# Optimization experiments

Hardware: AMD Instinct MI355X
Metric: run time of the kernel (lower is better)

Reference implementation:

```python
import jax, jax.numpy as jnp
import numpy as np

B, L, D, H = 4, 2048, 1024, 16
HD = D // H
NEG = -1e9  # stands in for -inf in masks; identical softmax result, grad-safe
EPS = 1e-5


def _layer_norm(x, g, b):
    mu = jnp.mean(x, axis=-1, keepdims=True)
    var = jnp.mean((x - mu) ** 2, axis=-1, keepdims=True)
    return (x - mu) * jax.lax.rsqrt(var + EPS) * g + b


def setup_inputs() -> dict:
    key = jax.random.key(0)
    ks = jax.random.split(key, 8)
    x = jax.random.normal(ks[0], (B, L, D), dtype=jnp.float32)
    # length-based padding: valid lengths in [L//2, L]; True = padded position
    lengths = jax.random.randint(ks[1], (B,), L // 2, L + 1)
    padding_mask = jnp.arange(L)[None, :] >= lengths[:, None]  # (B, L) bool
    # additive causal mask: 0 on/below diagonal, NEG above
    causal_mask = jnp.where(jnp.tril(jnp.ones((L, L), dtype=bool)), 0.0, NEG).astype(jnp.float32)

    def linear_params(k, fan_in, fan_out):
        bound = float(np.sqrt(6.0 / (fan_in + fan_out)))  # xavier_uniform
        W = jax.random.uniform(k, (fan_out, fan_in), jnp.float32, -bound, bound)
        b = jnp.zeros((fan_out,), jnp.float32)
        return W, b

    Wq, bq = linear_params(ks[2], D, D)
    Wk, bk = linear_params(ks[3], D, D)
    Wv, bv = linear_params(ks[4], D, D)
    Wo, bo = linear_params(ks[5], D, D)
    g_pre = jnp.ones((D,), jnp.float32); b_pre = jnp.zeros((D,), jnp.float32)
    g_ln = jnp.ones((D,), jnp.float32); b_ln = jnp.zeros((D,), jnp.float32)
    return {
        "x": x, "padding_mask": padding_mask, "causal_mask": causal_mask,
        "Wq": Wq, "bq": bq, "Wk": Wk, "bk": bk, "Wv": Wv, "bv": bv,
        "Wo": Wo, "bo": bo, "g_pre": g_pre, "b_pre": b_pre,
        "g_ln": g_ln, "b_ln": b_ln,
    }


def reference(x, padding_mask, causal_mask, Wq, bq, Wk, bk, Wv, bv, Wo, bo,
              g_pre, b_pre, g_ln, b_ln):
    # pre-LayerNorm (residual uses the normed x, matching the torch code)
    h = _layer_norm(x, g_pre, b_pre)  # (B, L, D)

    def heads(W, b):
        y = jnp.einsum('bld,ed->ble', h, W) + b           # torch Linear: x @ W.T + b
        return y.reshape(B, L, H, HD).transpose(0, 2, 1, 3)  # (B, H, L, HD)

    q, k, v = heads(Wq, bq), heads(Wk, bk), heads(Wv, bv)

    scores = jnp.einsum('bhld,bhmd->bhlm', q, k) / jnp.sqrt(jnp.float32(HD))
    scores = scores + causal_mask  # additive causal mask broadcast over (B, H)
    # padding mask: True = masked key position
    scores = jnp.where(padding_mask[:, None, None, :], NEG, scores)
    attn = jax.nn.softmax(scores, axis=-1)  # dropout p=0.0 (eval / disabled)

    out = jnp.einsum('bhlm,bhmd->bhld', attn, v)          # (B, H, L, HD)
    out = out.transpose(0, 2, 1, 3).reshape(B, L, D)
    out = jnp.einsum('bld,ed->ble', out, Wo) + bo
    return _layer_norm(out + h, g_ln, b_ln)
```

## Files before the change

kernel.cpp:

```cpp
#include <hip/hip_runtime.h>


#define Bq 4
#define Lq 2048
#define Dq 1024
#define Hq 16
#define HDq 64
#define Mq (Bq * Lq)

typedef __attribute__((ext_vector_type(8))) short short8;
typedef __attribute__((ext_vector_type(4))) float f32x4;
typedef __attribute__((address_space(3))) unsigned char lds_byte;
typedef __attribute__((address_space(1))) unsigned char gbl_byte;

__device__ __forceinline__ unsigned short f2b(float f) {
    unsigned int u = __float_as_uint(f);
    unsigned int r = (u + 0x7fffu + ((u >> 16) & 1u)) >> 16;
    return (unsigned short)r;
}
__device__ __forceinline__ float b2f(unsigned short u) {
    return __uint_as_float(((unsigned int)u) << 16);
}
__device__ __forceinline__ unsigned int packbf(float lo, float hi) {
    return (unsigned int)f2b(lo) | ((unsigned int)f2b(hi) << 16);
}

#define GLL16(gsrc, ldst)                                              \
    __builtin_amdgcn_global_load_lds((const gbl_byte*)(gsrc),          \
                                     (lds_byte*)(ldst), 16, 0, 0)

#define MFMA_BF16(A, B, C) \
    __builtin_amdgcn_mfma_f32_16x16x32_bf16((A), (B), (C), 0, 0, 0)

__global__ void setup_kernel(const unsigned char* __restrict__ m8,
                             int* __restrict__ lengths) {
    __shared__ int bad;
    __shared__ int fo[4];
    const int tid = threadIdx.x;
    if (tid == 0) bad = 0;
    if (tid < 4) fo[tid] = Lq;
    __syncthreads();
    for (int i = tid; i < Bq * Lq; i += 256) {
        unsigned char v = m8[i];
        if (v) {
            int r = i >> 11, c = i & (Lq - 1);
            atomicMin(&fo[r], c);
            if (c < Lq / 2) atomicOr(&bad, 1);
            else if (c < Lq - 1 && m8[i + 1] == 0) atomicOr(&bad, 1);
        }
    }
    __syncthreads();
    int anyone = (fo[0] < Lq) | (fo[1] < Lq) | (fo[2] < Lq) | (fo[3] < Lq);
    bool use8 = (bad == 0) && anyone;
    if (!use8) {
        __syncthreads();
        if (tid < 4) fo[tid] = Lq;
        __syncthreads();
        const int* m32 = (const int*)m8;
        for (int i = tid; i < Bq * Lq; i += 256) {
            if (m32[i] != 0) atomicMin(&fo[i >> 11], i & (Lq - 1));
        }
        __syncthreads();
    }
    if (tid < 4) lengths[tid] = fo[tid];
}

__global__ __launch_bounds__(256) void cvt4_kernel(
    const float* __restrict__ s0, const float* __restrict__ s1,
    const float* __restrict__ s2, const float* __restrict__ s3,
    unsigned short* __restrict__ dst) {
    const int region = blockIdx.x >> 10;
    const int i = (blockIdx.x & 1023) * 256 + threadIdx.x;
    const float* src = (region == 0) ? s0 : (region == 1) ? s1
                       : (region == 2) ? s2 : s3;
    float4 v = ((const float4*)src)[i];
    ushort4 o;
    o.x = f2b(v.x); o.y = f2b(v.y); o.z = f2b(v.z); o.w = f2b(v.w);
    ((ushort4*)dst)[(size_t)region * (Dq * Dq / 4) + i] = o;
}

__global__ __launch_bounds__(256) void ln_pre_kernel(
    const float* __restrict__ x, const float* __restrict__ g,
    const float* __restrict__ bb, unsigned short* __restrict__ out) {
    const int row = blockIdx.x, tid = threadIdx.x;
    float4 u = ((const float4*)x)[(size_t)row * 256 + tid];
    float s = u.x + u.y + u.z + u.w;
    float ss = u.x * u.x + u.y * u.y + u.z * u.z + u.w * u.w;
#pragma unroll
    for (int off = 32; off > 0; off >>= 1) {
        s += __shfl_xor(s, off);
        ss += __shfl_xor(ss, off);
    }
    __shared__ float sred[4], ssred[4];
    const int w = tid >> 6, lane = tid & 63;
    if (lane == 0) { sred[w] = s; ssred[w] = ss; }
    __syncthreads();
    s = sred[0] + sred[1] + sred[2] + sred[3];
    ss = ssred[0] + ssred[1] + ssred[2] + ssred[3];
    const float mean = s * (1.f / Dq);
    const float rstd = rsqrtf(ss * (1.f / Dq) - mean * mean + 1e-5f);
    float4 gv = ((const float4*)g)[tid];
    float4 bv = ((const float4*)bb)[tid];
    ushort4 o;
    o.x = f2b((u.x - mean) * rstd * gv.x + bv.x);
    o.y = f2b((u.y - mean) * rstd * gv.y + bv.y);
    o.z = f2b((u.z - mean) * rstd * gv.z + bv.z);
    o.w = f2b((u.w - mean) * rstd * gv.w + bv.w);
    ((ushort4*)out)[(size_t)row * 256 + tid] = o;
}

__global__ __launch_bounds__(256) void qkv_gemm_kernel(
    const unsigned short* __restrict__ A, const unsigned short* __restrict__ W3,
    const float* __restrict__ bq, const float* __restrict__ bk,
    const float* __restrict__ bv, unsigned short* __restrict__ Qo,
    unsigned short* __restrict__ Ko, unsigned short* __restrict__ Vto) {
    __shared__ unsigned short As[128][32];
    __shared__ unsigned short Bs[128][32];
    const int tid = threadIdx.x;
    const int w = tid >> 6, lane = tid & 63;
    const int lm = lane & 15, lq = lane >> 4;
    const int lin = blockIdx.y * 24 + blockIdx.x;
    const int swz = (lin & 7) * (1536 / 8) + (lin >> 3);
    const int m0 = (swz / 24) << 7, n0 = (swz % 24) << 7;
    const int wm = (w >> 1) << 6, wn = (w & 1) << 6;
    f32x4 acc[4][4];
#pragma unroll
    for (int i = 0; i < 4; ++i)
#pragma unroll
        for (int j = 0; j < 4; ++j) acc[i][j] = (f32x4){0.f, 0.f, 0.f, 0.f};
    for (int k0 = 0; k0 < Dq; k0 += 32) {
        __syncthreads();
#pragma unroll
        for (int j = 0; j < 2; ++j) {
            const int base = j * 256 + w * 64;
            const int slot = base + lane;
            const int row = slot >> 2, c = slot & 3;
            GLL16(A + (size_t)(m0 + row) * Dq + k0 + c * 8,
                  (unsigned short*)As + base * 8);
            GLL16(W3 + (size_t)(n0 + row) * Dq + k0 + c * 8,
                  (unsigned short*)Bs + base * 8);
        }
        __syncthreads();
        short8 af[4], bf[4];
#pragma unroll
        for (int t = 0; t < 4; ++t)
            af[t] = *(const short8*)&As[wm + t * 16 + lm][lq * 8];
#pragma unroll
        for (int t = 0; t < 4; ++t)
            bf[t] = *(const short8*)&Bs[wn + t * 16 + lm][lq * 8];
#pragma unroll
        for (int mt = 0; mt < 4; ++mt)
#pragma unroll
            for (int nt = 0; nt < 4; ++nt)
                acc[mt][nt] = __builtin_amdgcn_mfma_f32_16x16x32_bf16(
                    af[mt], bf[nt], acc[mt][nt], 0, 0, 0);
    }
    const int region = n0 >> 10;
    const float* bias = (region == 0) ? bq : (region == 1) ? bk : bv;
    const float scale = (region == 0) ? 0.125f : 1.0f;
    const int nb = n0 & 1023;
#pragma unroll
    for (int nt = 0; nt < 4; ++nt) {
        const int colb = nb + wn + nt * 16 + lm;
        const float bval = bias[colb];
#pragma unroll
        for (int mt = 0; mt < 4; ++mt) {
            const int row0 = m0 + wm + mt * 16 + lq * 4;
            const int bidx = row0 >> 11, l0r = row0 & (Lq - 1);
            if (region < 2) {
                unsigned short* dst = (region == 0) ? Qo : Ko;
#pragma unroll
                for (int r = 0; r < 4; ++r)
                    dst[((size_t)(bidx * Hq + (colb >> 6)) * Lq + l0r + r) *
                            HDq + (colb & 63)] =
                        f2b((acc[mt][nt][r] + bval) * scale);
            } else {
                ushort4 o;
                o.x = f2b(acc[mt][nt][0] + bval);
                o.y = f2b(acc[mt][nt][1] + bval);
                o.z = f2b(acc[mt][nt][2] + bval);
                o.w = f2b(acc[mt][nt][3] + bval);
                *(ushort4*)&Vto[((size_t)(bidx * Hq + (colb >> 6)) * HDq +
                                 (colb & 63)) * Lq + l0r] = o;
            }
        }
    }
}

__global__ __launch_bounds__(256) void proj_gemm_kernel(
    const unsigned short* __restrict__ A, const unsigned short* __restrict__ Bw,
    const float* __restrict__ bias, float* __restrict__ Cout) {
    __shared__ unsigned short As[128][32];
    __shared__ unsigned short Bs[128][32];
    const int tid = threadIdx.x;
    const int w = tid >> 6, lane = tid & 63;
    const int lm = lane & 15, lq = lane >> 4;
    const int lin = blockIdx.y * 8 + blockIdx.x;
    const int swz = (lin & 7) * (512 / 8) + (lin >> 3);
    const int m0 = (swz >> 3) << 7, n0 = (swz & 7) << 7;
    const int wm = (w >> 1) << 6, wn = (w & 1) << 6;
    f32x4 acc[4][4];
#pragma unroll
    for (int i = 0; i < 4; ++i)
#pragma unroll
        for (int j = 0; j < 4; ++j) acc[i][j] = (f32x4){0.f, 0.f, 0.f, 0.f};
    for (int k0 = 0; k0 < Dq; k0 += 32) {
        __syncthreads();
#pragma unroll
        for (int j = 0; j < 2; ++j) {
            const int base = j * 256 + w * 64;
            const int slot = base + lane;
            const int row = slot >> 2, c = slot & 3;
            const int rr = m0 + row, kk = k0 + c * 8;
            GLL16(A + ((size_t)((rr >> 11) * Hq + (kk >> 6)) * Lq +
                       (rr & (Lq - 1))) * HDq + (kk & 63),
                  (unsigned short*)As + base * 8);
            GLL16(Bw + (size_t)(n0 + row) * Dq + k0 + c * 8,
                  (unsigned short*)Bs + base * 8);
        }
        __syncthreads();
        short8 af[4], bf[4];
#pragma unroll
        for (int t = 0; t < 4; ++t)
            af[t] = *(const short8*)&As[wm + t * 16 + lm][lq * 8];
#pragma unroll
        for (int t = 0; t < 4; ++t)
            bf[t] = *(const short8*)&Bs[wn + t * 16 + lm][lq * 8];
#pragma unroll
        for (int mt = 0; mt < 4; ++mt)
#pragma unroll
            for (int nt = 0; nt < 4; ++nt)
                acc[mt][nt] = __builtin_amdgcn_mfma_f32_16x16x32_bf16(
                    af[mt], bf[nt], acc[mt][nt], 0, 0, 0);
    }
#pragma unroll
    for (int nt = 0; nt < 4; ++nt) {
        const float bval = bias[n0 + wn + nt * 16 + lm];
#pragma unroll
        for (int mt = 0; mt < 4; ++mt)
#pragma unroll
            for (int r = 0; r < 4; ++r)
                Cout[(size_t)(m0 + wm + mt * 16 + lq * 4 + r) * Dq + n0 + wn +
                     nt * 16 + lm] = acc[mt][nt][r] + bval;
    }
}

__global__ __launch_bounds__(256, 2) void attn_kernel(
    const unsigned short* __restrict__ Qg, const unsigned short* __restrict__ Kg,
    const unsigned short* __restrict__ Vtg, const int* __restrict__ lengths,
    unsigned short* __restrict__ Og) {
    __shared__ unsigned short Kbuf[2][4096];
    __shared__ unsigned short Vbuf[2][4096];
    __shared__ unsigned short Ps[4][2][16][72];
    const int bx = blockIdx.x;
    const int hh = blockIdx.y, b = blockIdx.z;
    const int tid = threadIdx.x, w = tid >> 6, lane = tid & 63;
    const int lm = lane & 15, lq = lane >> 4;
    const int len = lengths[b];
    const int mxk = (len + 63) >> 6;
    const size_t hb = (size_t)(b * Hq + hh) * Lq * HDq;
    const unsigned short* Vb = Vtg + hb;

    const int srow = w * 8 + (lane >> 3);
    const int ssw = (lane & 7) ^ (lane >> 3);
    const unsigned short* pK = Kg + hb + (size_t)srow * HDq + ssw * 8;
    const unsigned short* pV = Vb + (size_t)srow * Lq + ssw * 8;

#define STAGE_KV(BUF, KB)                                                   \
    {                                                                       \
        GLL16(pK + (size_t)(KB)*HDq, &Kbuf[(BUF)][(w * 64) * 8]);           \
        GLL16(pK + (size_t)((KB) + 32) * HDq,                               \
              &Kbuf[(BUF)][(256 + w * 64) * 8]);                            \
        GLL16(pV + (KB), &Vbuf[(BUF)][(w * 64) * 8]);                       \
        GLL16(pV + (size_t)32 * Lq + (KB),                                  \
              &Vbuf[(BUF)][(256 + w * 64) * 8]);                            \
    }

#pragma unroll
    for (int pass = 0; pass < 2; ++pass) {
        const int qt = pass ? bx : (15 - bx);
        const int l0 = qt << 7;
        short8 qf[2][2];
#pragma unroll
        for (int s = 0; s < 2; ++s)
#pragma unroll
            for (int h = 0; h < 2; ++h)
                qf[s][h] = *(const short8*)(Qg + hb +
                    (size_t)(l0 + w * 32 + s * 16 + lm) * HDq + h * 32 + lq * 8);
        f32x4 oacc[2][4];
        float m_i[2], l_i[2];
#pragma unroll
        for (int s = 0; s < 2; ++s) {
            m_i[s] = -1e30f; l_i[s] = 0.f;
#pragma unroll
            for (int t = 0; t < 4; ++t)
                oacc[s][t] = (f32x4){0.f, 0.f, 0.f, 0.f};
        }
        int nkt = 2 * qt + 2;
        if (nkt > mxk) nkt = mxk;
        STAGE_KV(0, 0);
        __syncthreads();
        for (int kt = 0; kt < nkt; ++kt) {
            const int kb = kt << 6;
            const int cur = kt & 1;
            if (kt + 1 < nkt) STAGE_KV(cur ^ 1, (kt + 1) << 6);
            short8 kf[4][2], vf[4][2];
#pragma unroll
            for (int t = 0; t < 4; ++t) {
                const int ro = (t * 16 + lm) * 64;
                const int sx = lm & 7;
#pragma unroll
                for (int h = 0; h < 2; ++h) {
                    const int off = ro + (((h * 4 + lq) ^ sx) << 3);
                    kf[t][h] = *(const short8*)&Kbuf[cur][off];
                    vf[t][h] = *(const short8*)&Vbuf[cur][off];
                }
            }
            f32x4 sc[2][4];
            __builtin_amdgcn_s_setprio(1);
#pragma unroll
            for (int s = 0; s < 2; ++s) {
#pragma unroll
                for (int t = 0; t < 4; ++t) {
                    f32x4 z = (f32x4){0.f, 0.f, 0.f, 0.f};
                    z = MFMA_BF16(kf[t][0], qf[s][0], z);
                    z = MFMA_BF16(kf[t][1], qf[s][1], z);
                    sc[s][t] = z;
                }
            }
            __builtin_amdgcn_s_setprio(0);
#pragma unroll
            for (int s = 0; s < 2; ++s) {
                const int qmin = l0 + w * 32 + s * 16;
                float pvv[16];
                float mx = -1e30f;
                if ((kb + 63 <= qmin) && (kb + 63 < len)) {
#pragma unroll
                    for (int i = 0; i < 16; ++i) {
                        const float v = sc[s][i >> 2][i & 3];
                        pvv[i] = v;
                        mx = fmaxf(mx, v);
                    }
                } else {
                    const int qq = qmin + lm;
#pragma unroll
                    for (int t = 0; t < 4; ++t)
#pragma unroll
                        for (int r = 0; r < 4; ++r) {
                            const int key = kb + t * 16 + lq * 4 + r;
                            float v = sc[s][t][r];
                            if (key > qq || key >= len) v = -1e30f;
                            pvv[t * 4 + r] = v;
                            mx = fmaxf(mx, v);
                        }
                }
                mx = fmaxf(mx, __shfl_xor(mx, 16));
                mx = fmaxf(mx, __shfl_xor(mx, 32));
                const float mnew = fmaxf(m_i[s], mx);
                float psum = 0.f;
#pragma unroll
                for (int i = 0; i < 16; ++i) {
                    const float p = __expf(pvv[i] - mnew);
                    pvv[i] = p;
                    psum += p;
                }
#pragma unroll
                for (int t = 0; t < 4; ++t) {
                    uint2 uu;
                    uu.x = packbf(pvv[t * 4 + 0], pvv[t * 4 + 1]);
                    uu.y = packbf(pvv[t * 4 + 2], pvv[t * 4 + 3]);
                    *(uint2*)&Ps[w][s][lm][t * 16 + lq * 4] = uu;
                }
                psum += __shfl_xor(psum, 16);
                psum += __shfl_xor(psum, 32);
                const float alpha = __expf(m_i[s] - mnew);
                m_i[s] = mnew;
                l_i[s] = l_i[s] * alpha + psum;
#pragma unroll
                for (int t = 0; t < 4; ++t) {
                    oacc[s][t][0] *= alpha; oacc[s][t][1] *= alpha;
                    oacc[s][t][2] *= alpha; oacc[s][t][3] *= alpha;
                }
            }
            asm volatile("s_waitcnt lgkmcnt(0)" ::: "memory");
            __builtin_amdgcn_s_setprio(1);
#pragma unroll
            for (int s = 0; s < 2; ++s) {
                short8 pf0 = *(const short8*)&Ps[w][s][lm][lq * 8];
                short8 pf1 = *(const short8*)&Ps[w][s][lm][32 + lq * 8];
#pragma unroll
                for (int t = 0; t < 4; ++t) {
                    oacc[s][t] = MFMA_BF16(vf[t][0], pf0, oacc[s][t]);
                    oacc[s][t] = MFMA_BF16(vf[t][1], pf1, oacc[s][t]);
                }
            }
            __builtin_amdgcn_s_setprio(0);
            __syncthreads();
        }
#pragma unroll
        for (int s = 0; s < 2; ++s) {
            const float inv = 1.f / l_i[s];
            unsigned short* Ot =
                Og + hb + (size_t)(l0 + w * 32 + s * 16 + lm) * HDq;
#pragma unroll
            for (int t = 0; t < 4; ++t) {
                ushort4 o;
                o.x = f2b(oacc[s][t][0] * inv);
                o.y = f2b(oacc[s][t][1] * inv);
                o.z = f2b(oacc[s][t][2] * inv);
                o.w = f2b(oacc[s][t][3] * inv);
                *(ushort4*)(Ot + t * 16 + lq * 4) = o;
            }
        }
    }
#undef STAGE_KV
}

__global__ __launch_bounds__(256) void ln_final_kernel(
    const float* __restrict__ pj, const unsigned short* __restrict__ h,
    const float* __restrict__ g, const float* __restrict__ bb,
    float* __restrict__ out) {
    const int row = blockIdx.x, tid = threadIdx.x;
    float4 a = ((const float4*)pj)[(size_t)row * 256 + tid];
    ushort4 hv = ((const ushort4*)h)[(size_t)row * 256 + tid];
    float f0 = a.x + b2f(hv.x), f1 = a.y + b2f(hv.y);
    float f2 = a.z + b2f(hv.z), f3 = a.w + b2f(hv.w);
    float s = f0 + f1 + f2 + f3;
    float ss = f0 * f0 + f1 * f1 + f2 * f2 + f3 * f3;
#pragma unroll
    for (int off = 32; off > 0; off >>= 1) {
        s += __shfl_xor(s, off);
        ss += __shfl_xor(ss, off);
    }
    __shared__ float sred[4], ssred[4];
    const int w = tid >> 6, lane = tid & 63;
    if (lane == 0) { sred[w] = s; ssred[w] = ss; }
    __syncthreads();
    s = sred[0] + sred[1] + sred[2] + sred[3];
    ss = ssred[0] + ssred[1] + ssred[2] + ssred[3];
    const float mean = s * (1.f / Dq);
    const float rstd = rsqrtf(ss * (1.f / Dq) - mean * mean + 1e-5f);
    float4 gv = ((const float4*)g)[tid];
    float4 bv = ((const float4*)bb)[tid];
    float4 o;
    o.x = (f0 - mean) * rstd * gv.x + bv.x;
    o.y = (f1 - mean) * rstd * gv.y + bv.y;
    o.z = (f2 - mean) * rstd * gv.z + bv.z;
    o.w = (f3 - mean) * rstd * gv.w + bv.w;
    ((float4*)out)[(size_t)row * 256 + tid] = o;
}

extern "C" void kernel_launch(void* const* d_in, const int* in_sizes, int n_in,
                              void* d_out, int out_size, void* d_ws,
                              size_t ws_size, hipStream_t stream) {
    const float* x = (const float*)d_in[0];
    const unsigned char* mask = (const unsigned char*)d_in[1];
    const float* Wq = (const float*)d_in[3];
    const float* bq = (const float*)d_in[4];
    const float* Wk = (const float*)d_in[5];
    const float* bk = (const float*)d_in[6];
    const float* Wv = (const float*)d_in[7];
    const float* bvv = (const float*)d_in[8];
    const float* Wo = (const float*)d_in[9];
    const float* bo = (const float*)d_in[10];
    const float* g_pre = (const float*)d_in[11];
    const float* b_pre = (const float*)d_in[12];
    const float* g_ln = (const float*)d_in[13];
    const float* b_ln = (const float*)d_in[14];

    const size_t SZ = (size_t)Mq * Dq;
    const size_t WSZ = (size_t)Dq * Dq;
    unsigned short* h = (unsigned short*)d_ws;
    unsigned short* q = h + SZ;
    unsigned short* k = q + SZ;
    unsigned short* vT = k + SZ;
    unsigned short* at = vT + SZ;
    unsigned short* W3 = at + SZ;
    unsigned short* wob = W3 + 3 * WSZ;
    float* proj = (float*)(wob + WSZ);
    int* lengths = (int*)(proj + SZ);

    setup_kernel<<<1, 256, 0, stream>>>(mask, lengths);
    cvt4_kernel<<<4096, 256, 0, stream>>>(Wq, Wk, Wv, Wo, W3);
    ln_pre_kernel<<<Mq, 256, 0, stream>>>(x, g_pre, b_pre, h);

    qkv_gemm_kernel<<<dim3(3 * Dq / 128, Mq / 128), 256, 0, stream>>>(
        h, W3, bq, bk, bvv, q, k, vT);
    attn_kernel<<<dim3(Lq / 256, Hq, Bq), 256, 0, stream>>>(q, k, vT, lengths,
                                                            at);
    proj_gemm_kernel<<<dim3(Dq / 128, Mq / 128), 256, 0, stream>>>(at, wob, bo,
                                                                   proj);
    ln_final_kernel<<<Mq, 256, 0, stream>>>(proj, h, g_ln, b_ln,
                                            (float*)d_out);
}
```

Baseline: 360.7 us.

## Double-buffer GEMM LDS tiles and remap attention blocks for XCD locality

Both the QKV and output-projection GEMMs now use two LDS buffers: the next K-slice is loaded asynchronously while MFMAs run on the current one, leaving one barrier per iteration instead of two. The attention kernel remaps its linear block index so that blocks sharing a (batch, head) land on the same XCD, which is meant to improve L2 reuse of K/V. Double buffering doubles the GEMM LDS footprint, which could reduce occupancy. The one-barrier scheme depends on the asynchronous global-to-LDS loads completing before the barrier.

```diff
diff --git a/kernel.cpp b/kernel.cpp
--- a/kernel.cpp
+++ b/kernel.cpp
@@ -114,8 +114,8 @@
     const float* __restrict__ bq, const float* __restrict__ bk,
     const float* __restrict__ bv, unsigned short* __restrict__ Qo,
     unsigned short* __restrict__ Ko, unsigned short* __restrict__ Vto) {
-    __shared__ unsigned short As[128][32];
-    __shared__ unsigned short Bs[128][32];
+    __shared__ unsigned short As[2][128][32];
+    __shared__ unsigned short Bs[2][128][32];
     const int tid = threadIdx.x;
     const int w = tid >> 6, lane = tid & 63;
     const int lm = lane & 15, lq = lane >> 4;
@@ -128,33 +128,42 @@
     for (int i = 0; i < 4; ++i)
 #pragma unroll
         for (int j = 0; j < 4; ++j) acc[i][j] = (f32x4){0.f, 0.f, 0.f, 0.f};
+
+#define QKV_STAGE(BUF, K0)                                              \
+    {                                                                   \
+        _Pragma("unroll")                                               \
+        for (int j = 0; j < 2; ++j) {                                   \
+            const int base = j * 256 + w * 64;                          \
+            const int slot = base + lane;                               \
+            const int row = slot >> 2, c = slot & 3;                    \
+            GLL16(A + (size_t)(m0 + row) * Dq + (K0) + c * 8,           \
+                  (unsigned short*)As[BUF] + base * 8);                 \
+            GLL16(W3 + (size_t)(n0 + row) * Dq + (K0) + c * 8,          \
+                  (unsigned short*)Bs[BUF] + base * 8);                 \
+        }                                                               \
+    }
+
+    QKV_STAGE(0, 0);
+    __syncthreads();
     for (int k0 = 0; k0 < Dq; k0 += 32) {
-        __syncthreads();
-#pragma unroll
-        for (int j = 0; j < 2; ++j) {
-            const int base = j * 256 + w * 64;
-            const int slot = base + lane;
-            const int row = slot >> 2, c = slot & 3;
-            GLL16(A + (size_t)(m0 + row) * Dq + k0 + c * 8,
-                  (unsigned short*)As + base * 8);
-            GLL16(W3 + (size_t)(n0 + row) * Dq + k0 + c * 8,
-                  (unsigned short*)Bs + base * 8);
-        }
-        __syncthreads();
+        const int cur = (k0 >> 5) & 1;
+        if (k0 + 32 < Dq) QKV_STAGE(cur ^ 1, k0 + 32);
         short8 af[4], bf[4];
 #pragma unroll
         for (int t = 0; t < 4; ++t)
-            af[t] = *(const short8*)&As[wm + t * 16 + lm][lq * 8];
+            af[t] = *(const short8*)&As[cur][wm + t * 16 + lm][lq * 8];
 #pragma unroll
         for (int t = 0; t < 4; ++t)
-            bf[t] = *(const short8*)&Bs[wn + t * 16 + lm][lq * 8];
+            bf[t] = *(const short8*)&Bs[cur][wn + t * 16 + lm][lq * 8];
 #pragma unroll
         for (int mt = 0; mt < 4; ++mt)
 #pragma unroll
             for (int nt = 0; nt < 4; ++nt)
                 acc[mt][nt] = __builtin_amdgcn_mfma_f32_16x16x32_bf16(
                     af[mt], bf[nt], acc[mt][nt], 0, 0, 0);
-    }
+        __syncthreads();
+    }
+#undef QKV_STAGE
     const int region = n0 >> 10;
     const float* bias = (region == 0) ? bq : (region == 1) ? bk : bv;
     const float scale = (region == 0) ? 0.125f : 1.0f;
@@ -190,8 +199,8 @@
 __global__ __launch_bounds__(256) void proj_gemm_kernel(
     const unsigned short* __restrict__ A, const unsigned short* __restrict__ Bw,
     const float* __restrict__ bias, float* __restrict__ Cout) {
-    __shared__ unsigned short As[128][32];
-    __shared__ unsigned short Bs[128][32];
+    __shared__ unsigned short As[2][128][32];
+    __shared__ unsigned short Bs[2][128][32];
     const int tid = threadIdx.x;
     const int w = tid >> 6, lane = tid & 63;
     const int lm = lane & 15, lq = lane >> 4;
@@ -204,35 +213,44 @@
     for (int i = 0; i < 4; ++i)
 #pragma unroll
         for (int j = 0; j < 4; ++j) acc[i][j] = (f32x4){0.f, 0.f, 0.f, 0.f};
+
+#define PROJ_STAGE(BUF, K0)                                             \
+    {                                                                   \
+        _Pragma("unroll")                                               \
+        for (int j = 0; j < 2; ++j) {                                   \
+            const int base = j * 256 + w * 64;                          \
+            const int slot = base + lane;                               \
+            const int row = slot >> 2, c = slot & 3;                    \
+            const int rr = m0 + row, kk = (K0) + c * 8;                 \
+            GLL16(A + ((size_t)((rr >> 11) * Hq + (kk >> 6)) * Lq +     \
+                       (rr & (Lq - 1))) * HDq + (kk & 63),              \
+                  (unsigned short*)As[BUF] + base * 8);                 \
+            GLL16(Bw + (size_t)(n0 + row) * Dq + (K0) + c * 8,          \
+                  (unsigned short*)Bs[BUF] + base * 8);                 \
+        }                                                               \
+    }
+
+    PROJ_STAGE(0, 0);
+    __syncthreads();
     for (int k0 = 0; k0 < Dq; k0 += 32) {
-        __syncthreads();
-#pragma unroll
-        for (int j = 0; j < 2; ++j) {
-            const int base = j * 256 + w * 64;
-            const int slot = base + lane;
-            const int row = slot >> 2, c = slot & 3;
-            const int rr = m0 + row, kk = k0 + c * 8;
-            GLL16(A + ((size_t)((rr >> 11) * Hq + (kk >> 6)) * Lq +
-                       (rr & (Lq - 1))) * HDq + (kk & 63),
-                  (unsigned short*)As + base * 8);
-            GLL16(Bw + (size_t)(n0 + row) * Dq + k0 + c * 8,
-                  (unsigned short*)Bs + base * 8);
-        }
-        __syncthreads();
+        const int cur = (k0 >> 5) & 1;
+        if (k0 + 32 < Dq) PROJ_STAGE(cur ^ 1, k0 + 32);
         short8 af[4], bf[4];
 #pragma unroll
         for (int t = 0; t < 4; ++t)
-            af[t] = *(const short8*)&As[wm + t * 16 + lm][lq * 8];
+            af[t] = *(const short8*)&As[cur][wm + t * 16 + lm][lq * 8];
 #pragma unroll
         for (int t = 0; t < 4; ++t)
-            bf[t] = *(const short8*)&Bs[wn + t * 16 + lm][lq * 8];
+            bf[t] = *(const short8*)&Bs[cur][wn + t * 16 + lm][lq * 8];
 #pragma unroll
         for (int mt = 0; mt < 4; ++mt)
 #pragma unroll
             for (int nt = 0; nt < 4; ++nt)
                 acc[mt][nt] = __builtin_amdgcn_mfma_f32_16x16x32_bf16(
                     af[mt], bf[nt], acc[mt][nt], 0, 0, 0);
-    }
+        __syncthreads();
+    }
+#undef PROJ_STAGE
 #pragma unroll
     for (int nt = 0; nt < 4; ++nt) {
         const float bval = bias[n0 + wn + nt * 16 + lm];
@@ -252,8 +270,11 @@
     __shared__ unsigned short Kbuf[2][4096];
     __shared__ unsigned short Vbuf[2][4096];
     __shared__ unsigned short Ps[4][2][16][72];
-    const int bx = blockIdx.x;
-    const int hh = blockIdx.y, b = blockIdx.z;
+    const int lin = blockIdx.x + (blockIdx.y << 3) + (blockIdx.z << 7);
+    const int xcd = lin & 7, sidx = lin >> 3;
+    const int grp = xcd * 8 + (sidx & 7);
+    const int bx = sidx >> 3;
+    const int hh = grp & 15, b = grp >> 4;
     const int tid = threadIdx.x, w = tid >> 6, lane = tid & 63;
     const int lm = lane & 15, lq = lane >> 4;
     const int len = lengths[b];
```

Measured after the change: 345.5 us. -4.2%, faster.
